# Kernel optimization log

Hardware: AMD Instinct MI355X
Metric: run time of the kernel (lower is better)

The kernel has to match this reference:

```python
import jax, jax.numpy as jnp
import numpy as np

B, N, C = 2, 512, 256


def setup_inputs() -> dict:
    key = jax.random.key(0)
    ks = jax.random.split(key, 6)
    s = 0.02
    return {
        "x": jax.random.normal(ks[0], (B, N, C), dtype=jnp.float32),
        "Wq": jax.random.normal(ks[1], (C, C), dtype=jnp.float32) * s,
        "Wk": jax.random.normal(ks[2], (C, C), dtype=jnp.float32) * s,
        "Wv": jax.random.normal(ks[3], (C, C), dtype=jnp.float32) * s,
        "Wp": jax.random.normal(ks[4], (C, C), dtype=jnp.float32) * s,
        "bp": jax.random.normal(ks[5], (C,), dtype=jnp.float32) * s,
    }


def reference(x, Wq, Wk, Wv, Wp, bp):
    # q,k,v: [B,N,C]; torch Linear(no bias) = x @ W.T
    q = jnp.einsum("bnc,dc->bnd", x, Wq)
    k = jnp.einsum("bnc,dc->bnd", x, Wk)
    v = jnp.einsum("bnc,dc->bnd", x, Wv)
    # additive score: sum_c relu(q_i + k_j)  -> [B,N,N]
    score = jax.nn.relu(q[:, :, None, :] + k[:, None, :, :]).sum(axis=-1)
    attn = jax.nn.softmax(score, axis=-1)  # [B,N,N] over keys j
    out = jnp.einsum("bij,bjc->bic", attn, v)  # weighted v sum
    out = jnp.einsum("bnc,dc->bnd", out, Wp) + bp  # proj (with bias)
    return out
```

## Files before the change

kernel.cpp:

```cpp
#include <hip/hip_runtime.h>
#include <hip/hip_bf16.h>


#define RFL(x) __builtin_amdgcn_readfirstlane(x)
#define QSTR 132

__global__ __launch_bounds__(256, 2) void gemm_qkv(
    const float* __restrict__ x,
    const float* __restrict__ Wq, const float* __restrict__ Wk, const float* __restrict__ Wv,
    float4* __restrict__ qt4, float* __restrict__ k, float* __restrict__ v,
    float* __restrict__ Ksp)
{
    const int z = blockIdx.z;
    const float* W = (z == 0) ? Wq : ((z == 1) ? Wk : Wv);
    const int row0 = blockIdx.x * 32;
    const int d0   = blockIdx.y * 64;

    __shared__ __attribute__((aligned(16))) float AT[32][36];
    __shared__ __attribute__((aligned(16))) float WT[32][68];

    const int tid = threadIdx.x;
    const int ty = tid >> 4, tx = tid & 15;

    float acc[2][4] = {};

    for (int c0 = 0; c0 < 256; c0 += 32) {
        {
            int r  = tid >> 3;
            int cb = (tid & 7) * 4;
            float4 a = *(const float4*)&x[(size_t)(row0 + r) * 256 + c0 + cb];
            AT[cb + 0][r] = a.x; AT[cb + 1][r] = a.y;
            AT[cb + 2][r] = a.z; AT[cb + 3][r] = a.w;
        }
        {
            int d  = tid >> 2;
            int cq = (tid & 3) * 8;
            float4 w0 = *(const float4*)&W[(size_t)(d0 + d) * 256 + c0 + cq];
            float4 w1 = *(const float4*)&W[(size_t)(d0 + d) * 256 + c0 + cq + 4];
            WT[cq + 0][d] = w0.x; WT[cq + 1][d] = w0.y;
            WT[cq + 2][d] = w0.z; WT[cq + 3][d] = w0.w;
            WT[cq + 4][d] = w1.x; WT[cq + 5][d] = w1.y;
            WT[cq + 6][d] = w1.z; WT[cq + 7][d] = w1.w;
        }
        __syncthreads();
#pragma unroll
        for (int c = 0; c < 32; ++c) {
            float2 a  = *(const float2*)&AT[c][ty * 2];
            float4 w4 = *(const float4*)&WT[c][tx * 4];
            acc[0][0] += a.x * w4.x; acc[0][1] += a.x * w4.y;
            acc[0][2] += a.x * w4.z; acc[0][3] += a.x * w4.w;
            acc[1][0] += a.y * w4.x; acc[1][1] += a.y * w4.y;
            acc[1][2] += a.y * w4.z; acc[1][3] += a.y * w4.w;
        }
        __syncthreads();
    }

    if (z == 0) {
#pragma unroll
        for (int rr = 0; rr < 2; ++rr)
            qt4[(size_t)(d0 / 4 + tx) * 1024 + row0 + ty * 2 + rr] =
                make_float4(acc[rr][0], acc[rr][1], acc[rr][2], acc[rr][3]);
    } else {
        float* out = (z == 1) ? k : v;
#pragma unroll
        for (int rr = 0; rr < 2; ++rr)
            *(float4*)&out[(size_t)(row0 + ty * 2 + rr) * 256 + d0 + tx * 4] =
                make_float4(acc[rr][0], acc[rr][1], acc[rr][2], acc[rr][3]);
        if (z == 1) {
#pragma unroll
            for (int rr = 0; rr < 2; ++rr) {
                float kp = acc[rr][0] + acc[rr][1] + acc[rr][2] + acc[rr][3];
#pragma unroll
                for (int d = 1; d < 16; d <<= 1) kp += __shfl_xor(kp, d, 16);
                if (tx == 0)
                    Ksp[(size_t)(d0 >> 6) * 1024 + row0 + ty * 2 + rr] = kp;
            }
        }
    }
}

__global__ __launch_bounds__(512, 2) void attn_partial(
    const float4* __restrict__ qt4, const float* __restrict__ kk,
    const float* __restrict__ vv, const float* __restrict__ Ksp,
    float* __restrict__ pacc, float* __restrict__ ml)
{
    const int it = blockIdx.x;
    const int js = blockIdx.y;
    const int b  = it >> 3;
    const int irow0 = it * 64;
    const int jrow0 = b * 512 + js * 32;

    __shared__ __attribute__((aligned(16))) float qbuf[64 * QSTR];
    __shared__ float sL[32][65];
    __shared__ float pl[32][65];

    const int t = threadIdx.x;
    const int w = t >> 6;
    const int l = t & 63;

    const int jbase = RFL(jrow0 + w * 4);
    const float* kw = kk + (size_t)jbase * 256;

    float s[4] = {0.f, 0.f, 0.f, 0.f};

    for (int h = 0; h < 2; ++h) {
#pragma unroll
        for (int u = 0; u < 4; ++u) {
            int idx = u * 512 + t;
            int c4 = idx >> 6, row = idx & 63;
            float4 a = qt4[(size_t)(h * 32 + c4) * 1024 + irow0 + row];
            *(float4*)&qbuf[row * QSTR + c4 * 4] = a;
        }
        __syncthreads();
        const float* kh = kw + h * 128;
        for (int c0 = 0; c0 < 128; c0 += 8) {
            float4 qa = *(const float4*)&qbuf[l * QSTR + c0];
            float4 qb = *(const float4*)&qbuf[l * QSTR + c0 + 4];
#pragma unroll
            for (int jj = 0; jj < 4; ++jj) {
                const float* kr = kh + jj * 256 + c0;
                s[jj] += fabsf(qa.x + kr[0]);
                s[jj] += fabsf(qa.y + kr[1]);
                s[jj] += fabsf(qa.z + kr[2]);
                s[jj] += fabsf(qa.w + kr[3]);
                s[jj] += fabsf(qb.x + kr[4]);
                s[jj] += fabsf(qb.y + kr[5]);
                s[jj] += fabsf(qb.z + kr[6]);
                s[jj] += fabsf(qb.w + kr[7]);
            }
        }
        __syncthreads();
    }

    float sc[4];
#pragma unroll
    for (int jj = 0; jj < 4; ++jj) {
        float ks = Ksp[jbase + jj] + Ksp[1024 + jbase + jj]
                 + Ksp[2048 + jbase + jj] + Ksp[3072 + jbase + jj];
        sc[jj] = 0.5f * (s[jj] + ks);
        sL[w * 4 + jj][l] = sc[jj];
    }
    __syncthreads();

    float m = -1e30f;
#pragma unroll
    for (int j = 0; j < 32; ++j) m = fmaxf(m, sL[j][l]);
#pragma unroll
    for (int jj = 0; jj < 4; ++jj)
        pl[w * 4 + jj][l] = __expf(sc[jj] - m);
    __syncthreads();

    if (w == 0) {
        float lsum = 0.f;
#pragma unroll
        for (int j = 0; j < 32; ++j) lsum += pl[j][l];
        *(float2*)&ml[((size_t)(irow0 + l) * 16 + js) * 2] = make_float2(m, lsum);
    }

    const int cb = w * 32;
    const float* vw = vv + (size_t)RFL(jrow0 * 256 + w * 32);
    float acc[32];
#pragma unroll
    for (int i = 0; i < 32; ++i) acc[i] = 0.f;
#pragma unroll 2
    for (int j = 0; j < 32; ++j) {
        float pj = pl[j][l];
#pragma unroll
        for (int cc = 0; cc < 32; ++cc)
            acc[cc] += pj * vw[j * 256 + cc];
    }
    float* pb = pacc + (((size_t)it * 16 + js) * 256 + cb) * 64 + l;
#pragma unroll
    for (int cc = 0; cc < 32; ++cc) pb[(size_t)cc * 64] = acc[cc];
}

__global__ __launch_bounds__(256) void combine(
    const float* __restrict__ pacc, const float* __restrict__ ml, float* __restrict__ OT)
{
    const int it = blockIdx.x;
    const int cs = blockIdx.y;
    const int t  = threadIdx.x;
    const int il = t & 63, cq = t >> 6;
    const int row = it * 64 + il;
    const int c0  = cs * 32 + cq * 8;

    float mv[16], lv[16], M = -1e30f;
#pragma unroll
    for (int s = 0; s < 16; ++s) {
        float2 e = *(const float2*)&ml[((size_t)row * 16 + s) * 2];
        mv[s] = e.x; lv[s] = e.y; M = fmaxf(M, e.x);
    }
    float L = 0.f;
    float o[8];
#pragma unroll
    for (int i = 0; i < 8; ++i) o[i] = 0.f;
#pragma unroll
    for (int s = 0; s < 16; ++s) {
        float wgt = __expf(mv[s] - M);
        L += wgt * lv[s];
        const float* pb = pacc + (((size_t)it * 16 + s) * 256 + c0) * 64 + il;
#pragma unroll
        for (int i = 0; i < 8; ++i) o[i] += wgt * pb[(size_t)i * 64];
    }
    float inv = 1.f / L;
#pragma unroll
    for (int i = 0; i < 8; ++i)
        OT[(size_t)(c0 + i) * 1024 + row] = o[i] * inv;
}

__global__ __launch_bounds__(256, 2) void gemm_bias(
    const float* __restrict__ OT, const float* __restrict__ W,
    const float* __restrict__ bias, float* __restrict__ out)
{
    const int row0 = blockIdx.x * 32;
    const int d0   = blockIdx.y * 64;

    __shared__ __attribute__((aligned(16))) float AT[32][36];
    __shared__ __attribute__((aligned(16))) float WT[32][68];

    const int tid = threadIdx.x;
    const int ty = tid >> 4, tx = tid & 15;

    float acc[2][4] = {};

    for (int c0 = 0; c0 < 256; c0 += 32) {
        {
            int cc = tid >> 3, r = (tid & 7) * 4;
            float4 a = *(const float4*)&OT[(size_t)(c0 + cc) * 1024 + row0 + r];
            *(float4*)&AT[cc][r] = a;
        }
        {
            int d  = tid >> 2;
            int cq = (tid & 3) * 8;
            float4 w0 = *(const float4*)&W[(size_t)(d0 + d) * 256 + c0 + cq];
            float4 w1 = *(const float4*)&W[(size_t)(d0 + d) * 256 + c0 + cq + 4];
            WT[cq + 0][d] = w0.x; WT[cq + 1][d] = w0.y;
            WT[cq + 2][d] = w0.z; WT[cq + 3][d] = w0.w;
            WT[cq + 4][d] = w1.x; WT[cq + 5][d] = w1.y;
            WT[cq + 6][d] = w1.z; WT[cq + 7][d] = w1.w;
        }
        __syncthreads();
#pragma unroll
        for (int c = 0; c < 32; ++c) {
            float2 a  = *(const float2*)&AT[c][ty * 2];
            float4 w4 = *(const float4*)&WT[c][tx * 4];
            acc[0][0] += a.x * w4.x; acc[0][1] += a.x * w4.y;
            acc[0][2] += a.x * w4.z; acc[0][3] += a.x * w4.w;
            acc[1][0] += a.y * w4.x; acc[1][1] += a.y * w4.y;
            acc[1][2] += a.y * w4.z; acc[1][3] += a.y * w4.w;
        }
        __syncthreads();
    }
    float4 bb = *(const float4*)&bias[d0 + tx * 4];
#pragma unroll
    for (int rr = 0; rr < 2; ++rr) {
        float4 o = make_float4(acc[rr][0] + bb.x, acc[rr][1] + bb.y,
                               acc[rr][2] + bb.z, acc[rr][3] + bb.w);
        *(float4*)&out[(size_t)(row0 + ty * 2 + rr) * 256 + d0 + tx * 4] = o;
    }
}

extern "C" void kernel_launch(void* const* d_in, const int* in_sizes, int n_in,
                              void* d_out, int out_size, void* d_ws, size_t ws_size,
                              hipStream_t stream) {
    const float* x  = (const float*)d_in[0];
    const float* Wq = (const float*)d_in[1];
    const float* Wk = (const float*)d_in[2];
    const float* Wv = (const float*)d_in[3];
    const float* Wp = (const float*)d_in[4];
    const float* bp = (const float*)d_in[5];
    float* out = (float*)d_out;
    (void)ws_size; (void)in_sizes; (void)n_in; (void)out_size;

    float* ws = (float*)d_ws;
    const size_t BNC = (size_t)2 * 512 * 256;
    float4* qt4 = (float4*)ws;
    float* k    = ws + BNC;
    float* v    = k + BNC;
    float* OT   = v + BNC;
    float* Ksp  = OT + BNC;
    float* pacc = Ksp + 4 * 1024;
    float* mlb  = pacc + (size_t)16 * 16 * 256 * 64;

    gemm_qkv<<<dim3(32, 4, 3), 256, 0, stream>>>(x, Wq, Wk, Wv, qt4, k, v, Ksp);
    attn_partial<<<dim3(16, 16), 512, 0, stream>>>(qt4, k, v, Ksp, pacc, mlb);
    combine<<<dim3(16, 8), 256, 0, stream>>>(pacc, mlb, OT);
    gemm_bias<<<dim3(32, 4), 256, 0, stream>>>(OT, Wp, bp, out);
}
```

Baseline: 67.96 us.

## Stage K and V tiles in LDS for attention; split combine across more blocks

In the attention-partial kernel, the K rows and V rows were read per wave with scalar loads straight from global memory. They are now staged cooperatively into shared memory, with V reusing the q buffer at a padded stride, and read back as float4 vectors. The launch bound is raised to request four blocks per CU. The combine kernel now gives each thread half as many channels and launches twice as many blocks to raise parallelism. The changes add one shared-memory K buffer plus extra LDS traffic, and may pressure registers under the tighter occupancy bound.

```diff
diff --git a/kernel.cpp b/kernel.cpp
--- a/kernel.cpp
+++ b/kernel.cpp
@@ -2,8 +2,8 @@
 #include <hip/hip_bf16.h>
 
 
-#define RFL(x) __builtin_amdgcn_readfirstlane(x)
 #define QSTR 132
+#define VSTR 260
 
 __global__ __launch_bounds__(256, 2) void gemm_qkv(
     const float* __restrict__ x,
@@ -79,7 +79,7 @@
     }
 }
 
-__global__ __launch_bounds__(512, 2) void attn_partial(
+__global__ __launch_bounds__(512, 4) void attn_partial(
     const float4* __restrict__ qt4, const float* __restrict__ kk,
     const float* __restrict__ vv, const float* __restrict__ Ksp,
     float* __restrict__ pacc, float* __restrict__ ml)
@@ -91,15 +91,14 @@
     const int jrow0 = b * 512 + js * 32;
 
     __shared__ __attribute__((aligned(16))) float qbuf[64 * QSTR];
+    __shared__ __attribute__((aligned(16))) float kbuf[32 * QSTR];
     __shared__ float sL[32][65];
     __shared__ float pl[32][65];
 
     const int t = threadIdx.x;
     const int w = t >> 6;
     const int l = t & 63;
-
-    const int jbase = RFL(jrow0 + w * 4);
-    const float* kw = kk + (size_t)jbase * 256;
+    const int j0 = w * 4;
 
     float s[4] = {0.f, 0.f, 0.f, 0.f};
 
@@ -111,34 +110,51 @@
             float4 a = qt4[(size_t)(h * 32 + c4) * 1024 + irow0 + row];
             *(float4*)&qbuf[row * QSTR + c4 * 4] = a;
         }
-        __syncthreads();
-        const float* kh = kw + h * 128;
+#pragma unroll
+        for (int u = 0; u < 2; ++u) {
+            int idx = u * 512 + t;
+            int row = idx >> 5, c4 = idx & 31;
+            float4 a = *(const float4*)&kk[(size_t)(jrow0 + row) * 256 + h * 128 + c4 * 4];
+            *(float4*)&kbuf[row * QSTR + c4 * 4] = a;
+        }
+        __syncthreads();
+
         for (int c0 = 0; c0 < 128; c0 += 8) {
             float4 qa = *(const float4*)&qbuf[l * QSTR + c0];
             float4 qb = *(const float4*)&qbuf[l * QSTR + c0 + 4];
 #pragma unroll
             for (int jj = 0; jj < 4; ++jj) {
-                const float* kr = kh + jj * 256 + c0;
-                s[jj] += fabsf(qa.x + kr[0]);
-                s[jj] += fabsf(qa.y + kr[1]);
-                s[jj] += fabsf(qa.z + kr[2]);
-                s[jj] += fabsf(qa.w + kr[3]);
-                s[jj] += fabsf(qb.x + kr[4]);
-                s[jj] += fabsf(qb.y + kr[5]);
-                s[jj] += fabsf(qb.z + kr[6]);
-                s[jj] += fabsf(qb.w + kr[7]);
+                float4 ka = *(const float4*)&kbuf[(j0 + jj) * QSTR + c0];
+                float4 kb = *(const float4*)&kbuf[(j0 + jj) * QSTR + c0 + 4];
+                s[jj] += fabsf(qa.x + ka.x);
+                s[jj] += fabsf(qa.y + ka.y);
+                s[jj] += fabsf(qa.z + ka.z);
+                s[jj] += fabsf(qa.w + ka.w);
+                s[jj] += fabsf(qb.x + kb.x);
+                s[jj] += fabsf(qb.y + kb.y);
+                s[jj] += fabsf(qb.z + kb.z);
+                s[jj] += fabsf(qb.w + kb.w);
             }
         }
         __syncthreads();
     }
 
+    const int jbase = jrow0 + j0;
     float sc[4];
 #pragma unroll
     for (int jj = 0; jj < 4; ++jj) {
         float ks = Ksp[jbase + jj] + Ksp[1024 + jbase + jj]
                  + Ksp[2048 + jbase + jj] + Ksp[3072 + jbase + jj];
         sc[jj] = 0.5f * (s[jj] + ks);
-        sL[w * 4 + jj][l] = sc[jj];
+        sL[j0 + jj][l] = sc[jj];
+    }
+
+#pragma unroll
+    for (int u = 0; u < 4; ++u) {
+        int idx = u * 512 + t;
+        int row = idx >> 6, c4 = idx & 63;
+        float4 a = *(const float4*)&vv[(size_t)(jrow0 + row) * 256 + c4 * 4];
+        *(float4*)&qbuf[row * VSTR + c4 * 4] = a;
     }
     __syncthreads();
 
@@ -147,7 +163,7 @@
     for (int j = 0; j < 32; ++j) m = fmaxf(m, sL[j][l]);
 #pragma unroll
     for (int jj = 0; jj < 4; ++jj)
-        pl[w * 4 + jj][l] = __expf(sc[jj] - m);
+        pl[j0 + jj][l] = __expf(sc[jj] - m);
     __syncthreads();
 
     if (w == 0) {
@@ -158,16 +174,19 @@
     }
 
     const int cb = w * 32;
-    const float* vw = vv + (size_t)RFL(jrow0 * 256 + w * 32);
     float acc[32];
 #pragma unroll
     for (int i = 0; i < 32; ++i) acc[i] = 0.f;
-#pragma unroll 2
     for (int j = 0; j < 32; ++j) {
         float pj = pl[j][l];
 #pragma unroll
-        for (int cc = 0; cc < 32; ++cc)
-            acc[cc] += pj * vw[j * 256 + cc];
+        for (int c4 = 0; c4 < 8; ++c4) {
+            float4 vv4 = *(const float4*)&qbuf[j * VSTR + cb + c4 * 4];
+            acc[c4 * 4 + 0] += pj * vv4.x;
+            acc[c4 * 4 + 1] += pj * vv4.y;
+            acc[c4 * 4 + 2] += pj * vv4.z;
+            acc[c4 * 4 + 3] += pj * vv4.w;
+        }
     }
     float* pb = pacc + (((size_t)it * 16 + js) * 256 + cb) * 64 + l;
 #pragma unroll
@@ -182,7 +201,7 @@
     const int t  = threadIdx.x;
     const int il = t & 63, cq = t >> 6;
     const int row = it * 64 + il;
-    const int c0  = cs * 32 + cq * 8;
+    const int c0  = cs * 16 + cq * 4;
 
     float mv[16], lv[16], M = -1e30f;
 #pragma unroll
@@ -191,20 +210,18 @@
         mv[s] = e.x; lv[s] = e.y; M = fmaxf(M, e.x);
     }
     float L = 0.f;
-    float o[8];
-#pragma unroll
-    for (int i = 0; i < 8; ++i) o[i] = 0.f;
+    float o[4] = {0.f, 0.f, 0.f, 0.f};
 #pragma unroll
     for (int s = 0; s < 16; ++s) {
         float wgt = __expf(mv[s] - M);
         L += wgt * lv[s];
         const float* pb = pacc + (((size_t)it * 16 + s) * 256 + c0) * 64 + il;
 #pragma unroll
-        for (int i = 0; i < 8; ++i) o[i] += wgt * pb[(size_t)i * 64];
+        for (int i = 0; i < 4; ++i) o[i] += wgt * pb[(size_t)i * 64];
     }
     float inv = 1.f / L;
 #pragma unroll
-    for (int i = 0; i < 8; ++i)
+    for (int i = 0; i < 4; ++i)
         OT[(size_t)(c0 + i) * 1024 + row] = o[i] * inv;
 }
 
@@ -284,6 +301,6 @@
 
     gemm_qkv<<<dim3(32, 4, 3), 256, 0, stream>>>(x, Wq, Wk, Wv, qt4, k, v, Ksp);
     attn_partial<<<dim3(16, 16), 512, 0, stream>>>(qt4, k, v, Ksp, pacc, mlb);
-    combine<<<dim3(16, 8), 256, 0, stream>>>(pacc, mlb, OT);
+    combine<<<dim3(16, 16), 256, 0, stream>>>(pacc, mlb, OT);
     gemm_bias<<<dim3(32, 4), 256, 0, stream>>>(OT, Wp, bp, out);
 }
```

Result: slower. 191.4 us (+181.6%).
